# Kernel optimization log

Hardware: AMD Instinct MI355X
Metric: run time of the kernel (lower is better)

The kernel has to match this reference:

```python
import jax, jax.numpy as jnp
import numpy as np
from jax import lax

B, L, DM = 2, 1024, 1024
DIN, DSTATE, DCONV, DTRANK = 2048, 16, 4, 64


def setup_inputs() -> dict:
    key = jax.random.key(0)
    ks = jax.random.split(key, 8)
    s = 0.02
    x = jax.random.normal(ks[0], (B, L, DM), jnp.float32)
    in_proj_w = jax.random.normal(ks[1], (2 * DIN, DM), jnp.float32) * s
    conv_w = jax.random.normal(ks[2], (DIN, 1, DCONV), jnp.float32) * 0.2
    conv_b = jnp.zeros((DIN,), jnp.float32)
    x_proj_w = jax.random.normal(ks[3], (DTRANK + 2 * DSTATE, DIN), jnp.float32) * s
    dt_proj_w = jax.random.normal(ks[4], (DIN, DTRANK), jnp.float32) * s
    dt_proj_b = jnp.full((DIN,), -4.0, jnp.float32)  # small init dt after softplus
    # S4D-real init: A_log = log(1..d_state) per channel
    A_log = jnp.log(jnp.broadcast_to(jnp.arange(1, DSTATE + 1, dtype=jnp.float32), (DIN, DSTATE)))
    D_skip = jnp.ones((DIN,), jnp.float32)
    out_proj_w = jax.random.normal(ks[5], (DM, DIN), jnp.float32) * s
    return {
        "x": x, "norm_w": jnp.ones((DM,), jnp.float32), "norm_b": jnp.zeros((DM,), jnp.float32),
        "in_proj_w": in_proj_w, "conv_w": conv_w, "conv_b": conv_b,
        "x_proj_w": x_proj_w, "dt_proj_w": dt_proj_w, "dt_proj_b": dt_proj_b,
        "A_log": A_log, "D_skip": D_skip, "out_proj_w": out_proj_w,
    }


def _layernorm(x, w, b, eps=1e-5):
    mu = jnp.mean(x, axis=-1, keepdims=True)
    var = jnp.mean(jnp.square(x - mu), axis=-1, keepdims=True)
    return (x - mu) * lax.rsqrt(var + eps) * w + b


def _mamba(h, in_proj_w, conv_w, conv_b, x_proj_w, dt_proj_w, dt_proj_b, A_log, D_skip, out_proj_w):
    # h: [B, L, DM]
    xz = jnp.einsum('bld,ed->ble', h, in_proj_w)          # [B, L, 2*DIN]
    xm, z = jnp.split(xz, 2, axis=-1)                     # each [B, L, DIN]
    # causal depthwise conv1d over time
    xc = jnp.transpose(xm, (0, 2, 1))                     # [B, DIN, L]
    xc = jnp.pad(xc, ((0, 0), (0, 0), (DCONV - 1, 0)))
    xc = lax.conv_general_dilated(xc, conv_w, (1,), 'VALID',
                                  dimension_numbers=('NCH', 'OIH', 'NCH'),
                                  feature_group_count=DIN)
    xc = xc + conv_b[None, :, None]
    xc = jnp.transpose(xc, (0, 2, 1))                     # [B, L, DIN]
    xc = jax.nn.silu(xc)
    # input-dependent SSM parameters
    x_dbl = jnp.einsum('bld,ed->ble', xc, x_proj_w)       # [B, L, DTRANK+2N]
    dt, Bm, Cm = jnp.split(x_dbl, [DTRANK, DTRANK + DSTATE], axis=-1)
    dt = jax.nn.softplus(jnp.einsum('blr,dr->bld', dt, dt_proj_w) + dt_proj_b)  # [B, L, DIN]
    A = -jnp.exp(A_log)                                   # [DIN, N]
    deltaA = jnp.exp(dt[..., None] * A)                   # [B, L, DIN, N]
    deltaBu = dt[..., None] * Bm[:, :, None, :] * xc[..., None]  # [B, L, DIN, N]
    # sequential selective scan over time
    dA_t = jnp.transpose(deltaA, (1, 0, 2, 3))            # [L, B, DIN, N]
    dBu_t = jnp.transpose(deltaBu, (1, 0, 2, 3))
    C_t = jnp.transpose(Cm, (1, 0, 2))                    # [L, B, N]

    def step(hs, inp):
        dA, dBu, Ct = inp
        hs = dA * hs + dBu                                # [B, DIN, N]
        y = jnp.einsum('bdn,bn->bd', hs, Ct)
        return hs, y

    h0 = jnp.zeros((B, DIN, DSTATE), xc.dtype)
    _, ys = lax.scan(step, h0, (dA_t, dBu_t, C_t))        # ys: [L, B, DIN]
    y = jnp.transpose(ys, (1, 0, 2)) + xc * D_skip        # [B, L, DIN]
    y = y * jax.nn.silu(z)
    return jnp.einsum('bld,ed->ble', y, out_proj_w)       # [B, L, DM]


def reference(x, norm_w, norm_b, in_proj_w, conv_w, conv_b, x_proj_w,
              dt_proj_w, dt_proj_b, A_log, D_skip, out_proj_w):
    h = _layernorm(x, norm_w, norm_b)
    return x + _mamba(h, in_proj_w, conv_w, conv_b, x_proj_w,
                      dt_proj_w, dt_proj_b, A_log, D_skip, out_proj_w)
```

## Files before the change

kernel.cpp:

```cpp
#include <hip/hip_runtime.h>


typedef unsigned short u16;
typedef unsigned int u32;

typedef __bf16 bf16x8 __attribute__((ext_vector_type(8)));
typedef float f32x4 __attribute__((ext_vector_type(4)));

#define SCAN_G 32
#define SCAN_T 32
#define NSTATE 65536

#if __has_builtin(__builtin_amdgcn_exp2f)
#define EXP2F(x) __builtin_amdgcn_exp2f(x)
#else
#define EXP2F(x) exp2f(x)
#endif
#define LOG2E 1.44269504f

__device__ __forceinline__ u16 f2bf(float f) {
  u32 u = __float_as_uint(f);
  u32 r = u + 0x7FFFu + ((u >> 16) & 1u);
  return (u16)(r >> 16);
}
__device__ __forceinline__ float bf2f(u16 v) {
  return __uint_as_float(((u32)v) << 16);
}

__device__ __forceinline__ void lds_load16(const u16* g, u16* l) {
  __builtin_amdgcn_global_load_lds(
      (const __attribute__((address_space(1))) u32*)g,
      (__attribute__((address_space(3))) u32*)l, 16, 0, 0);
}

__global__ __launch_bounds__(256) void convert_ln_kernel(
    const float* __restrict__ w0, const float* __restrict__ w1,
    const float* __restrict__ w2, const float* __restrict__ w3,
    u16* __restrict__ o0, u16* __restrict__ o1,
    u16* __restrict__ o2, u16* __restrict__ o3,
    const float* __restrict__ x, const float* __restrict__ nw,
    const float* __restrict__ nb, u16* __restrict__ h) {
  const int bx = blockIdx.x;
  const int tid = threadIdx.x;
  if (bx < 6464) {
    const int q = bx * 256 + tid;
    const float4* src;
    ushort4* dst;
    int off;
    if (q < 1048576) { src = (const float4*)w0; dst = (ushort4*)o0; off = q; }
    else if (q < 1097728) { src = (const float4*)w1; dst = (ushort4*)o1; off = q - 1048576; }
    else if (q < 1130496) { src = (const float4*)w2; dst = (ushort4*)o2; off = q - 1097728; }
    else { src = (const float4*)w3; dst = (ushort4*)o3; off = q - 1130496; }
    const float4 v = src[off];
    ushort4 o;
    o.x = f2bf(v.x); o.y = f2bf(v.y); o.z = f2bf(v.z); o.w = f2bf(v.w);
    dst[off] = o;
    return;
  }
  const int row = bx - 6464;
  const float4 v = ((const float4*)(x + (size_t)row * 1024))[tid];
  float s = v.x + v.y + v.z + v.w;
  float s2 = v.x * v.x + v.y * v.y + v.z * v.z + v.w * v.w;
  for (int off = 32; off >= 1; off >>= 1) {
    s += __shfl_xor(s, off);
    s2 += __shfl_xor(s2, off);
  }
  __shared__ float red[8];
  const int wave = tid >> 6;
  if ((tid & 63) == 0) { red[wave * 2] = s; red[wave * 2 + 1] = s2; }
  __syncthreads();
  s = red[0] + red[2] + red[4] + red[6];
  s2 = red[1] + red[3] + red[5] + red[7];
  const float mu = s * (1.0f / 1024.0f);
  const float var = s2 * (1.0f / 1024.0f) - mu * mu;
  const float rstd = rsqrtf(var + 1e-5f);
  const float4 wv = ((const float4*)nw)[tid];
  const float4 bv = ((const float4*)nb)[tid];
  ushort4 o;
  o.x = f2bf((v.x - mu) * rstd * wv.x + bv.x);
  o.y = f2bf((v.y - mu) * rstd * wv.y + bv.y);
  o.z = f2bf((v.z - mu) * rstd * wv.z + bv.z);
  o.w = f2bf((v.w - mu) * rstd * wv.w + bv.w);
  ((ushort4*)(h + (size_t)row * 1024))[tid] = o;
}

__global__ __launch_bounds__(256) void gemm128_kernel(
    const u16* __restrict__ A, const u16* __restrict__ W,
    u16* __restrict__ Cout, int M, int N, int K) {
  const int n0 = blockIdx.x * 128;
  const int m0 = blockIdx.y * 128;
  __shared__ u16 As[128 * 32];
  __shared__ u16 Ws[128 * 32];
  const int tid = threadIdx.x;
  const int wave = tid >> 6;
  const int lane = tid & 63;
  const int wm = (wave >> 1) * 64;
  const int wn = (wave & 1) * 64;
  f32x4 acc[4][4];
#pragma unroll
  for (int i = 0; i < 4; ++i)
#pragma unroll
    for (int j = 0; j < 4; ++j) acc[i][j] = (f32x4){0.f, 0.f, 0.f, 0.f};
  const int fm = lane & 15;
  const int fk = (lane >> 4) * 8;
  const int sr = lane >> 2;
  const int sc = (lane & 3) * 8;
  const u16* gA = A + (size_t)(m0 + wave * 32 + sr) * K + sc;
  const u16* gB = W + (size_t)(n0 + wave * 32 + sr) * K + sc;
  u16* lA = As + wave * 1024;
  u16* lB = Ws + wave * 1024;

  for (int kk = 0; kk < K; kk += 32) {
    __syncthreads();
    lds_load16(gA + kk, lA);
    lds_load16(gA + (size_t)16 * K + kk, lA + 512);
    lds_load16(gB + kk, lB);
    lds_load16(gB + (size_t)16 * K + kk, lB + 512);
    __syncthreads();
    bf16x8 af[4], bfr[4];
#pragma unroll
    for (int i = 0; i < 4; ++i)
      af[i] = *(const bf16x8*)(As + (wm + i * 16 + fm) * 32 + fk);
#pragma unroll
    for (int j = 0; j < 4; ++j)
      bfr[j] = *(const bf16x8*)(Ws + (wn + j * 16 + fm) * 32 + fk);
#pragma unroll
    for (int i = 0; i < 4; ++i)
#pragma unroll
      for (int j = 0; j < 4; ++j)
        acc[i][j] = __builtin_amdgcn_mfma_f32_16x16x32_bf16(af[i], bfr[j], acc[i][j], 0, 0, 0);
  }
  const int col = lane & 15;
  const int rb = (lane >> 4) * 4;
#pragma unroll
  for (int i = 0; i < 4; ++i)
#pragma unroll
    for (int j = 0; j < 4; ++j)
#pragma unroll
      for (int r = 0; r < 4; ++r) {
        const int m = m0 + wm + i * 16 + rb + r;
        const int n = n0 + wn + j * 16 + col;
        Cout[(size_t)m * N + n] = f2bf(acc[i][j][r]);
      }
}

__global__ __launch_bounds__(256) void conv_silu_kernel(
    const u16* __restrict__ xzb, const float* __restrict__ cw,
    const float* __restrict__ cb, u16* __restrict__ xcb) {
  const int idx = blockIdx.x * 256 + threadIdx.x;
  const int d = idx & 2047;
  const int m = idx >> 11;
  const int l = m & 1023;
  const float4 wv = ((const float4*)cw)[d];
  const float w4[4] = {wv.x, wv.y, wv.z, wv.w};
  float acc = cb[d];
#pragma unroll
  for (int k = 0; k < 4; ++k) {
    int lk = l + k - 3;
    if (lk >= 0) acc += bf2f(xzb[(size_t)(m + k - 3) * 4096 + d]) * w4[k];
  }
  const float sv = acc / (1.0f + __expf(-acc));
  xcb[idx] = f2bf(sv);
}

__global__ __launch_bounds__(256) void gemm_bt_kernel(
    const u16* __restrict__ A, const u16* __restrict__ W,
    float* __restrict__ C, int M, int N, int K) {
  const int n0 = blockIdx.x * 64;
  const int m0 = blockIdx.y * 64;
  const int ks = blockIdx.z;
  const int kLen = K / 4;
  const int kOff = ks * kLen;
  __shared__ u16 As[64 * 32];
  __shared__ u16 Ws[64 * 32];
  const int tid = threadIdx.x;
  const int wave = tid >> 6;
  const int lane = tid & 63;
  const int wm = (wave >> 1) * 32;
  const int wn = (wave & 1) * 32;
  const int lrow = tid >> 2;
  const int lcg = (tid & 3) * 8;
  f32x4 acc[2][2];
#pragma unroll
  for (int i = 0; i < 2; ++i)
#pragma unroll
    for (int j = 0; j < 2; ++j) acc[i][j] = (f32x4){0.f, 0.f, 0.f, 0.f};
  const int fm = lane & 15;
  const int fk = (lane >> 4) * 8;
  const int wrow = n0 + lrow;
  for (int k0 = kOff; k0 < kOff + kLen; k0 += 32) {
    uint4 av = *(const uint4*)(A + (size_t)(m0 + lrow) * K + k0 + lcg);
    uint4 wv = make_uint4(0u, 0u, 0u, 0u);
    if (wrow < N) wv = *(const uint4*)(W + (size_t)wrow * K + k0 + lcg);
    __syncthreads();
    *(uint4*)(As + lrow * 32 + lcg) = av;
    *(uint4*)(Ws + lrow * 32 + lcg) = wv;
    __syncthreads();
    bf16x8 a0 = *(const bf16x8*)(As + (wm + fm) * 32 + fk);
    bf16x8 a1 = *(const bf16x8*)(As + (wm + 16 + fm) * 32 + fk);
    bf16x8 b0 = *(const bf16x8*)(Ws + (wn + fm) * 32 + fk);
    bf16x8 b1 = *(const bf16x8*)(Ws + (wn + 16 + fm) * 32 + fk);
    acc[0][0] = __builtin_amdgcn_mfma_f32_16x16x32_bf16(a0, b0, acc[0][0], 0, 0, 0);
    acc[0][1] = __builtin_amdgcn_mfma_f32_16x16x32_bf16(a0, b1, acc[0][1], 0, 0, 0);
    acc[1][0] = __builtin_amdgcn_mfma_f32_16x16x32_bf16(a1, b0, acc[1][0], 0, 0, 0);
    acc[1][1] = __builtin_amdgcn_mfma_f32_16x16x32_bf16(a1, b1, acc[1][1], 0, 0, 0);
  }
  const int col = lane & 15;
  const int rbase = (lane >> 4) * 4;
#pragma unroll
  for (int tm = 0; tm < 2; ++tm)
#pragma unroll
    for (int tn = 0; tn < 2; ++tn)
#pragma unroll
      for (int r = 0; r < 4; ++r) {
        int m = m0 + wm + tm * 16 + rbase + r;
        int n = n0 + wn + tn * 16 + col;
        if (n < N)
          C[(size_t)ks * M * N + (size_t)m * N + n] = acc[tm][tn][r];
      }
}

__global__ __launch_bounds__(256) void dtgemm_fused_kernel(
    const float* __restrict__ xpart, const u16* __restrict__ Wdt,
    const float* __restrict__ bias, u16* __restrict__ dtb,
    float* __restrict__ xdbl) {
  const int N = 2048, K = 64;
  const int n0 = blockIdx.x * 64;
  const int m0 = blockIdx.y * 64;
  const int tid = threadIdx.x;
  if (blockIdx.x == 0) {
#pragma unroll
    for (int j = 0; j < 8; ++j) {
      const int e = tid * 8 + j;
      const size_t ix = (size_t)(m0 + (e >> 5)) * 96 + 64 + (e & 31);
      xdbl[ix] = xpart[ix] + xpart[ix + 196608] + xpart[ix + 2 * 196608] +
                 xpart[ix + 3 * 196608];
    }
  }
  __shared__ u16 As[64 * 32];
  __shared__ u16 Ws[64 * 32];
  const int wave = tid >> 6;
  const int lane = tid & 63;
  const int wm = (wave >> 1) * 32;
  const int wn = (wave & 1) * 32;
  const int lrow = tid >> 2;
  const int lcg = (tid & 3) * 8;
  f32x4 acc[2][2];
#pragma unroll
  for (int i = 0; i < 2; ++i)
#pragma unroll
    for (int j = 0; j < 2; ++j) acc[i][j] = (f32x4){0.f, 0.f, 0.f, 0.f};
  const int fm = lane & 15;
  const int fk = (lane >> 4) * 8;
  for (int k0 = 0; k0 < K; k0 += 32) {
    const size_t ab = (size_t)(m0 + lrow) * 96 + k0 + lcg;
    float av[8];
#pragma unroll
    for (int t = 0; t < 2; ++t) {
      float4 v0 = *(const float4*)&xpart[ab + t * 4];
      float4 v1 = *(const float4*)&xpart[ab + 196608 + t * 4];
      float4 v2 = *(const float4*)&xpart[ab + 2 * 196608 + t * 4];
      float4 v3 = *(const float4*)&xpart[ab + 3 * 196608 + t * 4];
      av[t * 4 + 0] = v0.x + v1.x + v2.x + v3.x;
      av[t * 4 + 1] = v0.y + v1.y + v2.y + v3.y;
      av[t * 4 + 2] = v0.z + v1.z + v2.z + v3.z;
      av[t * 4 + 3] = v0.w + v1.w + v2.w + v3.w;
    }
    ushort4 ap0, ap1;
    ap0.x = f2bf(av[0]); ap0.y = f2bf(av[1]); ap0.z = f2bf(av[2]); ap0.w = f2bf(av[3]);
    ap1.x = f2bf(av[4]); ap1.y = f2bf(av[5]); ap1.z = f2bf(av[6]); ap1.w = f2bf(av[7]);
    uint4 wv = *(const uint4*)(Wdt + (size_t)(n0 + lrow) * K + k0 + lcg);
    __syncthreads();
    *(ushort4*)(As + lrow * 32 + lcg) = ap0;
    *(ushort4*)(As + lrow * 32 + lcg + 4) = ap1;
    *(uint4*)(Ws + lrow * 32 + lcg) = wv;
    __syncthreads();
    bf16x8 a0 = *(const bf16x8*)(As + (wm + fm) * 32 + fk);
    bf16x8 a1 = *(const bf16x8*)(As + (wm + 16 + fm) * 32 + fk);
    bf16x8 b0 = *(const bf16x8*)(Ws + (wn + fm) * 32 + fk);
    bf16x8 b1 = *(const bf16x8*)(Ws + (wn + 16 + fm) * 32 + fk);
    acc[0][0] = __builtin_amdgcn_mfma_f32_16x16x32_bf16(a0, b0, acc[0][0], 0, 0, 0);
    acc[0][1] = __builtin_amdgcn_mfma_f32_16x16x32_bf16(a0, b1, acc[0][1], 0, 0, 0);
    acc[1][0] = __builtin_amdgcn_mfma_f32_16x16x32_bf16(a1, b0, acc[1][0], 0, 0, 0);
    acc[1][1] = __builtin_amdgcn_mfma_f32_16x16x32_bf16(a1, b1, acc[1][1], 0, 0, 0);
  }
  const int col = lane & 15;
  const int rbase = (lane >> 4) * 4;
#pragma unroll
  for (int tm = 0; tm < 2; ++tm)
#pragma unroll
    for (int tn = 0; tn < 2; ++tn)
#pragma unroll
      for (int r = 0; r < 4; ++r) {
        const int m = m0 + wm + tm * 16 + rbase + r;
        const int n = n0 + wn + tn * 16 + col;
        float v = acc[tm][tn][r] + bias[n];
        v = (v > 20.f) ? v : log1pf(__expf(v));
        dtb[(size_t)m * 2048 + n] = f2bf(v);
      }
}

__global__ __launch_bounds__(256) void scan_pass1_kernel(
    const u16* __restrict__ dtb, const u16* __restrict__ xcb,
    const float* __restrict__ xdbl, const float* __restrict__ A_log,
    float* __restrict__ hend, float* __restrict__ prodA) {
  const int bx = blockIdx.x;
  const int d0 = (bx & 7) * 256;
  const int b = (bx >> 3) & 1;
  const int g = bx >> 4;
  const int tid = threadIdx.x;
  const int d = d0 + tid;
  const int mb = b * 1024 + g * SCAN_T;
  float a2[16];
#pragma unroll
  for (int q = 0; q < 4; ++q) {
    float4 al = *(const float4*)&A_log[(size_t)d * 16 + q * 4];
    a2[q * 4 + 0] = -__expf(al.x) * LOG2E;
    a2[q * 4 + 1] = -__expf(al.y) * LOG2E;
    a2[q * 4 + 2] = -__expf(al.z) * LOG2E;
    a2[q * 4 + 3] = -__expf(al.w) * LOG2E;
  }
  float h[16];
#pragma unroll
  for (int n = 0; n < 16; ++n) h[n] = 0.f;
  float cs = 0.f;
  const u16* dp = dtb + (size_t)mb * 2048 + d;
  const u16* xp = xcb + (size_t)mb * 2048 + d;
  const float* xb = xdbl + (size_t)mb * 96 + 64;
#pragma unroll 4
  for (int s = 0; s < SCAN_T; ++s) {
    const float dtv = bf2f(dp[(size_t)s * 2048]);
    const float xcv = bf2f(xp[(size_t)s * 2048]);
    const float du = dtv * xcv;
    const float4 B0 = *(const float4*)(xb + (size_t)s * 96 + 0);
    const float4 B1 = *(const float4*)(xb + (size_t)s * 96 + 4);
    const float4 B2 = *(const float4*)(xb + (size_t)s * 96 + 8);
    const float4 B3 = *(const float4*)(xb + (size_t)s * 96 + 12);
    const float Bv[16] = {B0.x, B0.y, B0.z, B0.w, B1.x, B1.y, B1.z, B1.w,
                          B2.x, B2.y, B2.z, B2.w, B3.x, B3.y, B3.z, B3.w};
#pragma unroll
    for (int n = 0; n < 16; ++n) {
      const float da = EXP2F(dtv * a2[n]);
      h[n] = __builtin_fmaf(da, h[n], du * Bv[n]);
    }
    cs += dtv;
  }
  const size_t base = ((size_t)(g * 2 + b) * 2048 + d) * 16;
#pragma unroll
  for (int q = 0; q < 4; ++q) {
    float4 hv = {h[q * 4], h[q * 4 + 1], h[q * 4 + 2], h[q * 4 + 3]};
    *(float4*)&hend[base + q * 4] = hv;
    float4 pv = {EXP2F(a2[q * 4] * cs), EXP2F(a2[q * 4 + 1] * cs),
                 EXP2F(a2[q * 4 + 2] * cs), EXP2F(a2[q * 4 + 3] * cs)};
    *(float4*)&prodA[base + q * 4] = pv;
  }
}

__global__ __launch_bounds__(256) void scan_combine_kernel(
    const float* __restrict__ hend, const float* __restrict__ prodA,
    float* __restrict__ hinit) {
  const int sid = blockIdx.x * 256 + threadIdx.x;
  float H = 0.f;
#pragma unroll 8
  for (int g = 0; g < SCAN_G; ++g) {
    hinit[g * NSTATE + sid] = H;
    H = prodA[g * NSTATE + sid] * H + hend[g * NSTATE + sid];
  }
}

__global__ __launch_bounds__(256) void scan_pass2_kernel(
    const u16* __restrict__ dtb, const u16* __restrict__ xcb,
    const u16* __restrict__ xzb, const float* __restrict__ xdbl,
    const float* __restrict__ A_log, const float* __restrict__ Dsk,
    const float* __restrict__ hinit, u16* __restrict__ yb) {
  const int bx = blockIdx.x;
  const int d0 = (bx & 7) * 256;
  const int b = (bx >> 3) & 1;
  const int g = bx >> 4;
  const int tid = threadIdx.x;
  const int d = d0 + tid;
  const int mb = b * 1024 + g * SCAN_T;
  float a2[16];
#pragma unroll
  for (int q = 0; q < 4; ++q) {
    float4 al = *(const float4*)&A_log[(size_t)d * 16 + q * 4];
    a2[q * 4 + 0] = -__expf(al.x) * LOG2E;
    a2[q * 4 + 1] = -__expf(al.y) * LOG2E;
    a2[q * 4 + 2] = -__expf(al.z) * LOG2E;
    a2[q * 4 + 3] = -__expf(al.w) * LOG2E;
  }
  const float Dd = Dsk[d];
  float h[16];
  {
    const float* hi = hinit + ((size_t)(g * 2 + b) * 2048 + d) * 16;
#pragma unroll
    for (int q = 0; q < 4; ++q) {
      float4 hv = *(const float4*)(hi + q * 4);
      h[q * 4] = hv.x; h[q * 4 + 1] = hv.y; h[q * 4 + 2] = hv.z; h[q * 4 + 3] = hv.w;
    }
  }
  const u16* dp = dtb + (size_t)mb * 2048 + d;
  const u16* xp = xcb + (size_t)mb * 2048 + d;
  const u16* zp = xzb + (size_t)mb * 4096 + 2048 + d;
  const float* xb = xdbl + (size_t)mb * 96 + 64;
  u16* yp = yb + (size_t)mb * 2048 + d;
#pragma unroll 2
  for (int s = 0; s < SCAN_T; ++s) {
    const float dtv = bf2f(dp[(size_t)s * 2048]);
    const float xcv = bf2f(xp[(size_t)s * 2048]);
    const float du = dtv * xcv;
    const float4 B0 = *(const float4*)(xb + (size_t)s * 96 + 0);
    const float4 B1 = *(const float4*)(xb + (size_t)s * 96 + 4);
    const float4 B2 = *(const float4*)(xb + (size_t)s * 96 + 8);
    const float4 B3 = *(const float4*)(xb + (size_t)s * 96 + 12);
    const float4 C0 = *(const float4*)(xb + (size_t)s * 96 + 16);
    const float4 C1 = *(const float4*)(xb + (size_t)s * 96 + 20);
    const float4 C2 = *(const float4*)(xb + (size_t)s * 96 + 24);
    const float4 C3 = *(const float4*)(xb + (size_t)s * 96 + 28);
    const float Bv[16] = {B0.x, B0.y, B0.z, B0.w, B1.x, B1.y, B1.z, B1.w,
                          B2.x, B2.y, B2.z, B2.w, B3.x, B3.y, B3.z, B3.w};
    const float Cv[16] = {C0.x, C0.y, C0.z, C0.w, C1.x, C1.y, C1.z, C1.w,
                          C2.x, C2.y, C2.z, C2.w, C3.x, C3.y, C3.z, C3.w};
    float y = 0.f;
#pragma unroll
    for (int n = 0; n < 16; ++n) {
      const float da = EXP2F(dtv * a2[n]);
      h[n] = __builtin_fmaf(da, h[n], du * Bv[n]);
      y = __builtin_fmaf(h[n], Cv[n], y);
    }
    const float zv = bf2f(zp[(size_t)s * 4096]);
    const float sig = 1.0f / (1.0f + EXP2F(-zv * LOG2E));
    const float yv = (y + xcv * Dd) * (zv * sig);
    yp[(size_t)s * 2048] = f2bf(yv);
  }
}

__global__ __launch_bounds__(256) void gemm_out_kernel(
    const u16* __restrict__ A, const u16* __restrict__ W,
    const float* __restrict__ x, float* __restrict__ out) {
  const int K = 2048;
  const int n0 = blockIdx.x * 128;
  const int m0 = blockIdx.y * 64;
  __shared__ u16 As[64 * 32];
  __shared__ u16 Ws[128 * 32];
  const int tid = threadIdx.x;
  const int wave = tid >> 6;
  const int lane = tid & 63;
  const int wm = (wave >> 1) * 32;
  const int wn = (wave & 1) * 64;
  f32x4 acc[2][4];
#pragma unroll
  for (int i = 0; i < 2; ++i)
#pragma unroll
    for (int j = 0; j < 4; ++j) acc[i][j] = (f32x4){0.f, 0.f, 0.f, 0.f};
  const int fm = lane & 15;
  const int fk = (lane >> 4) * 8;
  const int sr = lane >> 2;
  const int sc = (lane & 3) * 8;
  const u16* gA = A + (size_t)(m0 + wave * 16 + sr) * K + sc;
  const u16* gB = W + (size_t)(n0 + wave * 32 + sr) * K + sc;
  u16* lA = As + wave * 512;
  u16* lB = Ws + wave * 1024;

  for (int kk = 0; kk < K; kk += 32) {
    __syncthreads();
    lds_load16(gA + kk, lA);
    lds_load16(gB + kk, lB);
    lds_load16(gB + (size_t)16 * K + kk, lB + 512);
    __syncthreads();
    bf16x8 af[2], bfr[4];
#pragma unroll
    for (int i = 0; i < 2; ++i)
      af[i] = *(const bf16x8*)(As + (wm + i * 16 + fm) * 32 + fk);
#pragma unroll
    for (int j = 0; j < 4; ++j)
      bfr[j] = *(const bf16x8*)(Ws + (wn + j * 16 + fm) * 32 + fk);
#pragma unroll
    for (int i = 0; i < 2; ++i)
#pragma unroll
      for (int j = 0; j < 4; ++j)
        acc[i][j] = __builtin_amdgcn_mfma_f32_16x16x32_bf16(af[i], bfr[j], acc[i][j], 0, 0, 0);
  }
  const int col = lane & 15;
  const int rb = (lane >> 4) * 4;
#pragma unroll
  for (int i = 0; i < 2; ++i)
#pragma unroll
    for (int j = 0; j < 4; ++j)
#pragma unroll
      for (int r = 0; r < 4; ++r) {
        const int m = m0 + wm + i * 16 + rb + r;
        const int n = n0 + wn + j * 16 + col;
        out[(size_t)m * 1024 + n] = x[(size_t)m * 1024 + n] + acc[i][j][r];
      }
}

extern "C" void kernel_launch(void* const* d_in, const int* in_sizes, int n_in,
                              void* d_out, int out_size, void* d_ws, size_t ws_size,
                              hipStream_t stream) {
  const float* x        = (const float*)d_in[0];
  const float* norm_w   = (const float*)d_in[1];
  const float* norm_b   = (const float*)d_in[2];
  const float* in_projw = (const float*)d_in[3];
  const float* conv_w   = (const float*)d_in[4];
  const float* conv_b   = (const float*)d_in[5];
  const float* x_projw  = (const float*)d_in[6];
  const float* dt_projw = (const float*)d_in[7];
  const float* dt_projb = (const float*)d_in[8];
  const float* A_log    = (const float*)d_in[9];
  const float* D_skip   = (const float*)d_in[10];
  const float* out_projw= (const float*)d_in[11];
  float* out = (float*)d_out;

  char* p = (char*)d_ws;
  auto alloc = [&](size_t bytes) {
    char* r = p;
    p += (bytes + 255) & ~(size_t)255;
    return r;
  };
  u16* xzb    = (u16*)alloc(2048ULL * 4096 * 2);
  u16* xcb    = (u16*)alloc(2048ULL * 2048 * 2);
  u16* dtb16  = (u16*)alloc(2048ULL * 2048 * 2);
  float* xdbl = (float*)alloc(2048ULL * 96 * 4);
  u16* h_bf   = (u16*)alloc(2048ULL * 1024 * 2);
  u16* ybf    = (u16*)alloc(2048ULL * 2048 * 2);
  u16* Wi     = (u16*)alloc(4096ULL * 1024 * 2);
  u16* Wx     = (u16*)alloc(96ULL * 2048 * 2);
  u16* Wdt    = (u16*)alloc(2048ULL * 64 * 2);
  u16* Wo     = (u16*)alloc(1024ULL * 2048 * 2);
  float* hend = (float*)alloc((size_t)SCAN_G * NSTATE * 4);
  float* prodA= (float*)alloc((size_t)SCAN_G * NSTATE * 4);
  float* hinit= (float*)alloc((size_t)SCAN_G * NSTATE * 4);
  float* xpart= (float*)alloc(4ULL * 2048 * 96 * 4);
  (void)ws_size; (void)in_sizes; (void)n_in; (void)out_size;

  convert_ln_kernel<<<8512, 256, 0, stream>>>(in_projw, x_projw, dt_projw,
                                              out_projw, Wi, Wx, Wdt, Wo,
                                              x, norm_w, norm_b, h_bf);

  gemm128_kernel<<<dim3(32, 16), 256, 0, stream>>>(h_bf, Wi, xzb, 2048, 4096, 1024);

  conv_silu_kernel<<<16384, 256, 0, stream>>>(xzb, conv_w, conv_b, xcb);

  gemm_bt_kernel<<<dim3(2, 32, 4), 256, 0, stream>>>(xcb, Wx, xpart, 2048, 96, 2048);

  dtgemm_fused_kernel<<<dim3(32, 32), 256, 0, stream>>>(xpart, Wdt, dt_projb,
                                                        dtb16, xdbl);

  scan_pass1_kernel<<<512, 256, 0, stream>>>(dtb16, xcb, xdbl, A_log, hend, prodA);
  scan_combine_kernel<<<256, 256, 0, stream>>>(hend, prodA, hinit);
  scan_pass2_kernel<<<512, 256, 0, stream>>>(dtb16, xcb, xzb, xdbl, A_log,
                                             D_skip, hinit, ybf);

  gemm_out_kernel<<<dim3(8, 32), 256, 0, stream>>>(ybf, Wo, x, out);
}
```

Before: 246.5 us.

## Split-K the output projection with bf16 partials and vectorize conv-silu

Replaces the output GEMM with a templated 128x128 GEMM run as 4-way split-K. It writes bf16 partial tiles into the reused xzb buffer, and a new combine kernel sums them with the residual. This aims to raise parallelism and tile reuse for the K=2048 projection, at the cost of an extra pass over the partials and bf16 rounding of the partial sums. The depthwise conv+SiLU kernel now handles four channels per thread with vector loads and stores.

Result: faster. 241.5 us (median of 2 runs) (-2.0%).

```diff
diff --git a/kernel.cpp b/kernel.cpp
--- a/kernel.cpp
+++ b/kernel.cpp
@@ -84,13 +84,9 @@
   ((ushort4*)(h + (size_t)row * 1024))[tid] = o;
 }
 
-__global__ __launch_bounds__(256) void gemm128_kernel(
-    const u16* __restrict__ A, const u16* __restrict__ W,
-    u16* __restrict__ Cout, int M, int N, int K) {
-  const int n0 = blockIdx.x * 128;
-  const int m0 = blockIdx.y * 128;
-  __shared__ u16 As[128 * 32];
-  __shared__ u16 Ws[128 * 32];
+__device__ __forceinline__ void gemm128_body(
+    const u16* A, const u16* W, u16* Cout, int N, int K,
+    int m0, int n0, int kOff, int kLen, size_t outBase, u16* As, u16* Ws) {
   const int tid = threadIdx.x;
   const int wave = tid >> 6;
   const int lane = tid & 63;
@@ -105,12 +101,12 @@
   const int fk = (lane >> 4) * 8;
   const int sr = lane >> 2;
   const int sc = (lane & 3) * 8;
-  const u16* gA = A + (size_t)(m0 + wave * 32 + sr) * K + sc;
-  const u16* gB = W + (size_t)(n0 + wave * 32 + sr) * K + sc;
+  const u16* gA = A + (size_t)(m0 + wave * 32 + sr) * K + kOff + sc;
+  const u16* gB = W + (size_t)(n0 + wave * 32 + sr) * K + kOff + sc;
   u16* lA = As + wave * 1024;
   u16* lB = Ws + wave * 1024;
 
-  for (int kk = 0; kk < K; kk += 32) {
+  for (int kk = 0; kk < kLen; kk += 32) {
     __syncthreads();
     lds_load16(gA + kk, lA);
     lds_load16(gA + (size_t)16 * K + kk, lA + 512);
@@ -140,27 +136,57 @@
       for (int r = 0; r < 4; ++r) {
         const int m = m0 + wm + i * 16 + rb + r;
         const int n = n0 + wn + j * 16 + col;
-        Cout[(size_t)m * N + n] = f2bf(acc[i][j][r]);
+        Cout[outBase + (size_t)m * N + n] = f2bf(acc[i][j][r]);
       }
+}
+
+template <int SPLITK>
+__global__ __launch_bounds__(256) void gemm128_kernel(
+    const u16* __restrict__ A, const u16* __restrict__ W,
+    u16* __restrict__ Cout, int M, int N, int K) {
+  const int n0 = blockIdx.x * 128;
+  const int m0 = blockIdx.y * 128;
+  const int ks = (SPLITK > 1) ? blockIdx.z : 0;
+  const int kLen = K / SPLITK;
+  __shared__ u16 As[128 * 32];
+  __shared__ u16 Ws[128 * 32];
+  gemm128_body(A, W, Cout, N, K, m0, n0, ks * kLen, kLen,
+               (SPLITK > 1) ? (size_t)ks * M * N : 0, As, Ws);
 }
 
 __global__ __launch_bounds__(256) void conv_silu_kernel(
     const u16* __restrict__ xzb, const float* __restrict__ cw,
     const float* __restrict__ cb, u16* __restrict__ xcb) {
-  const int idx = blockIdx.x * 256 + threadIdx.x;
-  const int d = idx & 2047;
-  const int m = idx >> 11;
+  const int u = blockIdx.x * 256 + threadIdx.x;
+  const int d4 = (u & 511) * 4;
+  const int m = u >> 9;
   const int l = m & 1023;
-  const float4 wv = ((const float4*)cw)[d];
-  const float w4[4] = {wv.x, wv.y, wv.z, wv.w};
-  float acc = cb[d];
+  const float4 wv0 = ((const float4*)cw)[d4];
+  const float4 wv1 = ((const float4*)cw)[d4 + 1];
+  const float4 wv2 = ((const float4*)cw)[d4 + 2];
+  const float4 wv3 = ((const float4*)cw)[d4 + 3];
+  const float4 cbv = ((const float4*)cb)[u & 511];
+  float a0 = cbv.x, a1 = cbv.y, a2 = cbv.z, a3 = cbv.w;
+  const float wk[4][4] = {{wv0.x, wv0.y, wv0.z, wv0.w},
+                          {wv1.x, wv1.y, wv1.z, wv1.w},
+                          {wv2.x, wv2.y, wv2.z, wv2.w},
+                          {wv3.x, wv3.y, wv3.z, wv3.w}};
 #pragma unroll
   for (int k = 0; k < 4; ++k) {
-    int lk = l + k - 3;
-    if (lk >= 0) acc += bf2f(xzb[(size_t)(m + k - 3) * 4096 + d]) * w4[k];
-  }
-  const float sv = acc / (1.0f + __expf(-acc));
-  xcb[idx] = f2bf(sv);
+    if (l + k - 3 >= 0) {
+      const ushort4 xv = *(const ushort4*)&xzb[(size_t)(m + k - 3) * 4096 + d4];
+      a0 += bf2f(xv.x) * wk[0][k];
+      a1 += bf2f(xv.y) * wk[1][k];
+      a2 += bf2f(xv.z) * wk[2][k];
+      a3 += bf2f(xv.w) * wk[3][k];
+    }
+  }
+  ushort4 o;
+  o.x = f2bf(a0 / (1.0f + __expf(-a0)));
+  o.y = f2bf(a1 / (1.0f + __expf(-a1)));
+  o.z = f2bf(a2 / (1.0f + __expf(-a2)));
+  o.w = f2bf(a3 / (1.0f + __expf(-a3)));
+  *(ushort4*)&xcb[(size_t)m * 2048 + d4] = o;
 }
 
 __global__ __launch_bounds__(256) void gemm_bt_kernel(
@@ -224,7 +250,7 @@
     const float* __restrict__ xpart, const u16* __restrict__ Wdt,
     const float* __restrict__ bias, u16* __restrict__ dtb,
     float* __restrict__ xdbl) {
-  const int N = 2048, K = 64;
+  const int K = 64;
   const int n0 = blockIdx.x * 64;
   const int m0 = blockIdx.y * 64;
   const int tid = threadIdx.x;
@@ -435,64 +461,19 @@
   }
 }
 
-__global__ __launch_bounds__(256) void gemm_out_kernel(
-    const u16* __restrict__ A, const u16* __restrict__ W,
-    const float* __restrict__ x, float* __restrict__ out) {
-  const int K = 2048;
-  const int n0 = blockIdx.x * 128;
-  const int m0 = blockIdx.y * 64;
-  __shared__ u16 As[64 * 32];
-  __shared__ u16 Ws[128 * 32];
-  const int tid = threadIdx.x;
-  const int wave = tid >> 6;
-  const int lane = tid & 63;
-  const int wm = (wave >> 1) * 32;
-  const int wn = (wave & 1) * 64;
-  f32x4 acc[2][4];
-#pragma unroll
-  for (int i = 0; i < 2; ++i)
-#pragma unroll
-    for (int j = 0; j < 4; ++j) acc[i][j] = (f32x4){0.f, 0.f, 0.f, 0.f};
-  const int fm = lane & 15;
-  const int fk = (lane >> 4) * 8;
-  const int sr = lane >> 2;
-  const int sc = (lane & 3) * 8;
-  const u16* gA = A + (size_t)(m0 + wave * 16 + sr) * K + sc;
-  const u16* gB = W + (size_t)(n0 + wave * 32 + sr) * K + sc;
-  u16* lA = As + wave * 512;
-  u16* lB = Ws + wave * 1024;
-
-  for (int kk = 0; kk < K; kk += 32) {
-    __syncthreads();
-    lds_load16(gA + kk, lA);
-    lds_load16(gB + kk, lB);
-    lds_load16(gB + (size_t)16 * K + kk, lB + 512);
-    __syncthreads();
-    bf16x8 af[2], bfr[4];
-#pragma unroll
-    for (int i = 0; i < 2; ++i)
-      af[i] = *(const bf16x8*)(As + (wm + i * 16 + fm) * 32 + fk);
-#pragma unroll
-    for (int j = 0; j < 4; ++j)
-      bfr[j] = *(const bf16x8*)(Ws + (wn + j * 16 + fm) * 32 + fk);
-#pragma unroll
-    for (int i = 0; i < 2; ++i)
-#pragma unroll
-      for (int j = 0; j < 4; ++j)
-        acc[i][j] = __builtin_amdgcn_mfma_f32_16x16x32_bf16(af[i], bfr[j], acc[i][j], 0, 0, 0);
-  }
-  const int col = lane & 15;
-  const int rb = (lane >> 4) * 4;
-#pragma unroll
-  for (int i = 0; i < 2; ++i)
-#pragma unroll
-    for (int j = 0; j < 4; ++j)
-#pragma unroll
-      for (int r = 0; r < 4; ++r) {
-        const int m = m0 + wm + i * 16 + rb + r;
-        const int n = n0 + wn + j * 16 + col;
-        out[(size_t)m * 1024 + n] = x[(size_t)m * 1024 + n] + acc[i][j][r];
-      }
+__global__ __launch_bounds__(256) void out_comb_kernel(
+    const u16* __restrict__ part, const float* __restrict__ x,
+    float* __restrict__ out) {
+  const int i4 = (blockIdx.x * 256 + threadIdx.x) * 4;
+  const float4 xv = *(const float4*)&x[i4];
+  float a0 = xv.x, a1 = xv.y, a2 = xv.z, a3 = xv.w;
+#pragma unroll
+  for (int ks = 0; ks < 4; ++ks) {
+    ushort4 pv = *(const ushort4*)&part[(size_t)ks * 2097152 + i4];
+    a0 += bf2f(pv.x); a1 += bf2f(pv.y); a2 += bf2f(pv.z); a3 += bf2f(pv.w);
+  }
+  float4 o = {a0, a1, a2, a3};
+  *(float4*)&out[i4] = o;
 }
 
 extern "C" void kernel_launch(void* const* d_in, const int* in_sizes, int n_in,
@@ -532,15 +513,16 @@
   float* prodA= (float*)alloc((size_t)SCAN_G * NSTATE * 4);
   float* hinit= (float*)alloc((size_t)SCAN_G * NSTATE * 4);
   float* xpart= (float*)alloc(4ULL * 2048 * 96 * 4);
+  u16* opart  = xzb;
   (void)ws_size; (void)in_sizes; (void)n_in; (void)out_size;
 
   convert_ln_kernel<<<8512, 256, 0, stream>>>(in_projw, x_projw, dt_projw,
                                               out_projw, Wi, Wx, Wdt, Wo,
                                               x, norm_w, norm_b, h_bf);
 
-  gemm128_kernel<<<dim3(32, 16), 256, 0, stream>>>(h_bf, Wi, xzb, 2048, 4096, 1024);
-
-  conv_silu_kernel<<<16384, 256, 0, stream>>>(xzb, conv_w, conv_b, xcb);
+  gemm128_kernel<1><<<dim3(32, 16), 256, 0, stream>>>(h_bf, Wi, xzb, 2048, 4096, 1024);
+
+  conv_silu_kernel<<<4096, 256, 0, stream>>>(xzb, conv_w, conv_b, xcb);
 
   gemm_bt_kernel<<<dim3(2, 32, 4), 256, 0, stream>>>(xcb, Wx, xpart, 2048, 96, 2048);
 
@@ -552,5 +534,6 @@
   scan_pass2_kernel<<<512, 256, 0, stream>>>(dtb16, xcb, xzb, xdbl, A_log,
                                              D_skip, hinit, ybf);
 
-  gemm_out_kernel<<<dim3(8, 32), 256, 0, stream>>>(ybf, Wo, x, out);
-}
+  gemm128_kernel<4><<<dim3(8, 16, 4), 256, 0, stream>>>(ybf, Wo, opart, 2048, 1024, 2048);
+  out_comb_kernel<<<2048, 256, 0, stream>>>(opart, x, out);
+}
```
